# Kernel tuning notes

Hardware: AMD Instinct MI355X
Metric: run time of the kernel (lower is better)

The kernel has to match this reference:

```python
import jax, jax.numpy as jnp
import numpy as np

T, B = 512, 256
OBS, H = 64, 512
M1, M2 = 512, 256


def setup_inputs() -> dict:
    key = jax.random.key(0)
    k = jax.random.split(key, 10)
    n = lambda i, shape, s=1.0: jax.random.normal(k[i], shape, dtype=jnp.float32) * s
    return {
        "x": n(0, (T * B, OBS)),
        "done": (jax.random.uniform(k[1], (T * B,)) < 0.05).astype(jnp.float32),
        "h0": n(2, (1, B, H), 0.1),
        "c0": n(3, (1, B, H), 0.1),
        "W_ih": n(4, (4 * H, OBS), OBS ** -0.5),
        "W_hh": n(5, (4 * H, H), H ** -0.5),
        "b_ih": jnp.zeros((4 * H,), jnp.float32),
        "b_hh": jnp.zeros((4 * H,), jnp.float32),
        "ln_g": jnp.ones((H,), jnp.float32),
        "ln_b": jnp.zeros((H,), jnp.float32),
        "W1": n(6, (M1, H), H ** -0.5),
        "b1": jnp.zeros((M1,), jnp.float32),
        "W2": n(7, (M2, M1), M1 ** -0.5),
        "b2": jnp.zeros((M2,), jnp.float32),
        "Wv": n(8, (1, M2), M2 ** -0.5),
        "bv": jnp.zeros((1,), jnp.float32),
    }


def _forward(x, done, h0, c0, W_ih, W_hh, b_ih, b_hh, ln_g, ln_b, W1, b1, W2, b2, Wv, bv):
    Bsz = h0.shape[1]
    obs = W_ih.shape[1]
    xs = x.reshape(-1, Bsz, obs)   # [T, B, obs]
    ds = done.reshape(-1, Bsz)     # [T, B]

    def step(carry, td):
        h, c = carry
        xt, dt = td
        m = (1.0 - dt)[:, None]    # done-based state reset, as in LSTMwithDones
        h = h * m
        c = c * m
        gates = xt @ W_ih.T + b_ih + h @ W_hh.T + b_hh  # [B, 4H]
        i, f, g, o = jnp.split(gates, 4, axis=-1)       # torch gate order i,f,g,o
        c = jax.nn.sigmoid(f) * c + jax.nn.sigmoid(i) * jnp.tanh(g)
        h = jax.nn.sigmoid(o) * jnp.tanh(c)
        return (h, c), h

    (hT, cT), hs = jax.lax.scan(step, (h0[0], c0[0]), (xs, ds))
    hidden = hs.reshape(-1, hs.shape[-1])  # flatten(cat(new_hidden), 0, 1) -> [T*B, H]

    # LayerNorm (eps = 1e-5, torch default)
    mu = hidden.mean(-1, keepdims=True)
    var = ((hidden - mu) ** 2).mean(-1, keepdims=True)
    hidden = (hidden - mu) * jax.lax.rsqrt(var + 1e-5) * ln_g + ln_b

    # MLP with tanh activation after every Linear (build_mlp appends act each layer)
    hmlp = jnp.tanh(hidden @ W1.T + b1)
    hmlp = jnp.tanh(hmlp @ W2.T + b2)
    value = hmlp @ Wv.T + bv               # [T*B, 1]
    return value, hT[None], cT[None]


def reference(x, done, h0, c0, W_ih, W_hh, b_ih, b_hh, ln_g, ln_b, W1, b1, W2, b2, Wv, bv):
    return _forward(x, done, h0, c0, W_ih, W_hh, b_ih, b_hh, ln_g, ln_b, W1, b1, W2, b2, Wv, bv)
```

## Files before the change

kernel.cpp:

```cpp
#include <hip/hip_runtime.h>
#include <stdint.h>

constexpr int T_STEPS = 512;
constexpr int BSZ     = 256;
constexpr int OBSD    = 64;
constexpr int HID     = 512;
constexpr int NROWS   = T_STEPS * BSZ;

constexpr int GROUPS = 16;
constexpr int WPG    = 16;
constexpr int BW     = 16;

typedef __attribute__((ext_vector_type(8))) short bf16x8;
typedef __attribute__((ext_vector_type(4))) float f32x4;

__device__ __forceinline__ float bf2f(uint16_t u) {
  union { uint32_t i; float f; } v; v.i = ((uint32_t)u) << 16; return v.f;
}
__device__ __forceinline__ uint16_t f2bf(float f) {
  union { float f; uint32_t i; } v; v.f = f;
  return (uint16_t)((v.i + 0x7FFFu + ((v.i >> 16) & 1u)) >> 16);
}
__device__ __forceinline__ uint64_t pack4(float a, float b, float c, float d) {
  uint32_t lo = (uint32_t)f2bf(a) | ((uint32_t)f2bf(b) << 16);
  uint32_t hi = (uint32_t)f2bf(c) | ((uint32_t)f2bf(d) << 16);
  return (uint64_t)lo | ((uint64_t)hi << 32);
}
__device__ __forceinline__ float sigm(float x) { return 1.f / (1.f + __expf(-x)); }
__device__ __forceinline__ float tanh_fast(float x) {
  float e = __expf(2.f * x);
  return 1.f - 2.f / (e + 1.f);
}

__device__ __forceinline__ void gll16(const void* g, void* l) {
  __builtin_amdgcn_global_load_lds(
      (const __attribute__((address_space(1))) uint32_t*)g,
      (__attribute__((address_space(3))) uint32_t*)l, 16, 0, 0);
}

__global__ __launch_bounds__(256, 1) void lstm_kernel(
    const float* __restrict__ xin, const float* __restrict__ done,
    const float* __restrict__ h0, const float* __restrict__ c0,
    const float* __restrict__ W_ih, const float* __restrict__ W_hh,
    const float* __restrict__ b_ih, const float* __restrict__ b_hh,
    uint16_t* __restrict__ hs, uint32_t* __restrict__ flg,
    float* __restrict__ out)
{
  __shared__ char  Ab[16 * 1152];
  __shared__ float gl[4 * 528];
  __shared__ float bl[128];

  const int wg   = blockIdx.x;
  const int g    = wg & 15;
  const int win  = wg >> 4;
  const int bg   = g * BW;
  const int tid  = threadIdx.x;
  const int lane = tid & 63;
  const int q    = tid >> 6;

  __builtin_amdgcn_fence(__ATOMIC_ACQUIRE, "agent");

  bf16x8 bq0[18], bq1[18];
  {
    const int r0  = q * 512 + win * 32 + (lane & 15);
    const int r1  = r0 + 16;
    const int kg8 = (lane >> 4) * 8;
    #pragma unroll
    for (int ks = 0; ks < 18; ++ks) {
      const float* s0 = (ks < 16)
          ? (W_hh + (size_t)r0 * 512 + ks * 32 + kg8)
          : (W_ih + (size_t)r0 * 64 + (ks - 16) * 32 + kg8);
      const float* s1 = (ks < 16)
          ? (W_hh + (size_t)r1 * 512 + ks * 32 + kg8)
          : (W_ih + (size_t)r1 * 64 + (ks - 16) * 32 + kg8);
      float4 a0 = *(const float4*)s0;
      float4 a1 = *(const float4*)(s0 + 4);
      float4 b0 = *(const float4*)s1;
      float4 b1 = *(const float4*)(s1 + 4);
      bf16x8 va, vb;
      va[0] = (short)f2bf(a0.x); va[1] = (short)f2bf(a0.y);
      va[2] = (short)f2bf(a0.z); va[3] = (short)f2bf(a0.w);
      va[4] = (short)f2bf(a1.x); va[5] = (short)f2bf(a1.y);
      va[6] = (short)f2bf(a1.z); va[7] = (short)f2bf(a1.w);
      vb[0] = (short)f2bf(b0.x); vb[1] = (short)f2bf(b0.y);
      vb[2] = (short)f2bf(b0.z); vb[3] = (short)f2bf(b0.w);
      vb[4] = (short)f2bf(b1.x); vb[5] = (short)f2bf(b1.y);
      vb[6] = (short)f2bf(b1.z); vb[7] = (short)f2bf(b1.w);
      bq0[ks] = va; bq1[ks] = vb;
    }
  }
  if (tid < 128) {
    int gq = tid >> 5, c = tid & 31;
    int grow = gq * 512 + win * 32 + c;
    bl[tid] = b_ih[grow] + b_hh[grow];
  }

  const int b_loc = tid >> 4;
  const int n0    = (tid & 15) * 2;
  float creg0 = c0[(size_t)(bg + b_loc) * HID + win * 32 + n0];
  float creg1 = c0[(size_t)(bg + b_loc) * HID + win * 32 + n0 + 1];

  const int sr  = tid >> 4;
  const int sc4 = (tid & 15) * 4;
  const int rw  = q * 4;

  __syncthreads();

  for (int t = 0; t < T_STEPS; ++t) {
    const float* xp = xin + ((size_t)t * BSZ + bg + sr) * OBSD + sc4;
    float4 xa = *(const float4*)xp;
    float dvs[4];
    #pragma unroll
    for (int r8 = 0; r8 < 4; ++r8)
      dvs[r8] = done[(size_t)t * BSZ + bg + rw + r8];
    float dv_b = done[(size_t)t * BSZ + bg + b_loc];

    *(uint64_t*)(Ab + ((sr * 1152 + 1024 + sc4 * 2) ^ ((sr & 7) << 4))) =
        pack4(xa.x, xa.y, xa.z, xa.w);

    if (t > 0) {
      for (;;) {
        uint32_t f = (lane < WPG)
            ? __hip_atomic_load(flg + g * 64 + q * 16 + lane,
                                __ATOMIC_RELAXED, __HIP_MEMORY_SCOPE_AGENT)
            : 0xFFFFFFFFu;
        if (__all((int)(f >= (uint32_t)t))) break;
        __builtin_amdgcn_s_sleep(1);
      }
      __builtin_amdgcn_fence(__ATOMIC_ACQUIRE, "workgroup");
    }

    if (t == 0) {
      #pragma unroll
      for (int r8 = 0; r8 < 4; ++r8) {
        int r = rw + r8;
        uint64_t v0 = 0, v1 = 0;
        if (dvs[r8] <= 0.5f) {
          const float* hp = h0 + (size_t)(bg + r) * HID;
          float4 ha = *(const float4*)(hp + lane * 4);
          float4 hb = *(const float4*)(hp + 256 + lane * 4);
          v0 = pack4(ha.x, ha.y, ha.z, ha.w);
          v1 = pack4(hb.x, hb.y, hb.z, hb.w);
        }
        *(uint64_t*)(Ab + ((r * 1152 + lane * 8) ^ ((r & 7) << 4))) = v0;
        *(uint64_t*)(Ab + ((r * 1152 + 512 + lane * 8) ^ ((r & 7) << 4))) = v1;
      }
    } else {
      #pragma unroll
      for (int r8 = 0; r8 < 4; ++r8) {
        int r = rw + r8;
        const uint4* hrow =
            (const uint4*)(hs + ((size_t)(t - 1) * BSZ + bg + r) * 512);
        uint4 v = hrow[lane];
        if (dvs[r8] > 0.5f) { v.x = 0; v.y = 0; v.z = 0; v.w = 0; }
        *(uint4*)(Ab + ((r * 1152 + lane * 16) ^ ((r & 7) << 4))) = v;
      }
    }
    __syncthreads();

    f32x4 ac0 = {0.f, 0.f, 0.f, 0.f};
    f32x4 ac1 = {0.f, 0.f, 0.f, 0.f};
    {
      const int ar = lane & 15;
      const int kg = lane >> 4;
      #pragma unroll
      for (int ks = 0; ks < 18; ++ks) {
        int kb = (ks * 32 + kg * 8) * 2;
        bf16x8 a = *(const bf16x8*)(Ab + ((ar * 1152 + kb) ^ ((ar & 7) << 4)));
        ac0 = __builtin_amdgcn_mfma_f32_16x16x32_bf16(a, bq0[ks], ac0, 0, 0, 0);
        ac1 = __builtin_amdgcn_mfma_f32_16x16x32_bf16(a, bq1[ks], ac1, 0, 0, 0);
      }
    }
    {
      int c  = lane & 15;
      int rb = (lane >> 4) * 4;
      #pragma unroll
      for (int r = 0; r < 4; ++r) {
        gl[q * 528 + (rb + r) * 33 + c]      = ac0[r];
        gl[q * 528 + (rb + r) * 33 + 16 + c] = ac1[r];
      }
    }
    __syncthreads();

    {
      float m = dv_b > 0.5f ? 0.f : 1.f;
      float h0v, h1v;
      {
        float I = gl[b_loc * 33 + n0]          + bl[n0];
        float F = gl[528 + b_loc * 33 + n0]    + bl[32 + n0];
        float G = gl[1056 + b_loc * 33 + n0]   + bl[64 + n0];
        float O = gl[1584 + b_loc * 33 + n0]   + bl[96 + n0];
        float cc = creg0 * m;
        cc = sigm(F) * cc + sigm(I) * tanh_fast(G);
        creg0 = cc;
        h0v = sigm(O) * tanh_fast(cc);
      }
      {
        int n1 = n0 + 1;
        float I = gl[b_loc * 33 + n1]          + bl[n1];
        float F = gl[528 + b_loc * 33 + n1]    + bl[32 + n1];
        float G = gl[1056 + b_loc * 33 + n1]   + bl[64 + n1];
        float O = gl[1584 + b_loc * 33 + n1]   + bl[96 + n1];
        float cc = creg1 * m;
        cc = sigm(F) * cc + sigm(I) * tanh_fast(G);
        creg1 = cc;
        h1v = sigm(O) * tanh_fast(cc);
      }
      uint32_t pk = (uint32_t)f2bf(h0v) | ((uint32_t)f2bf(h1v) << 16);
      uint32_t* hp = (uint32_t*)(hs + ((size_t)t * BSZ + bg + b_loc) * HID + win * 32 + n0);
      __hip_atomic_store(hp, pk, __ATOMIC_RELAXED, __HIP_MEMORY_SCOPE_AGENT);
      if (t == T_STEPS - 1) {
        size_t ob = (size_t)(bg + b_loc) * HID + win * 32 + n0;
        out[NROWS + ob]         = h0v;
        out[NROWS + ob + 1]     = h1v;
        out[2 * NROWS + ob]     = creg0;
        out[2 * NROWS + ob + 1] = creg1;
      }
    }
    asm volatile("s_waitcnt vmcnt(0)" ::: "memory");
    if ((tid & 63) == 0)
      __hip_atomic_store(flg + g * 64 + q * 16 + win, (uint32_t)(t + 1),
                         __ATOMIC_RELAXED, __HIP_MEMORY_SCOPE_AGENT);
  }
}

__global__ void uv_kernel(const float* __restrict__ W1, const float* __restrict__ ln_g,
                          const float* __restrict__ ln_b, const float* __restrict__ b1,
                          float* __restrict__ u, float* __restrict__ v)
{
  const int lane = threadIdx.x & 63;
  const int row  = blockIdx.x * 4 + (threadIdx.x >> 6);
  const float* wp = W1 + (size_t)row * 512 + lane * 8;
  float4 w0 = *(const float4*)wp;
  float4 w1 = *(const float4*)(wp + 4);
  float4 g0 = *(const float4*)(ln_g + lane * 8);
  float4 g1 = *(const float4*)(ln_g + lane * 8 + 4);
  float4 b0 = *(const float4*)(ln_b + lane * 8);
  float4 b1v = *(const float4*)(ln_b + lane * 8 + 4);
  float su = b0.x * w0.x + b0.y * w0.y + b0.z * w0.z + b0.w * w0.w
           + b1v.x * w1.x + b1v.y * w1.y + b1v.z * w1.z + b1v.w * w1.w;
  float sv = g0.x * w0.x + g0.y * w0.y + g0.z * w0.z + g0.w * w0.w
           + g1.x * w1.x + g1.y * w1.y + g1.z * w1.z + g1.w * w1.w;
  #pragma unroll
  for (int o = 1; o < 64; o <<= 1) { su += __shfl_xor(su, o); sv += __shfl_xor(sv, o); }
  if (lane == 0) { u[row] = su + b1[row]; v[row] = sv; }
}

template<int MODE>
__global__ __launch_bounds__(256, 2) void gemm_fused(
    const uint16_t* __restrict__ Abase, const uint16_t* __restrict__ W,
    uint16_t* __restrict__ C, int ntiles,
    const float* __restrict__ uvec, const float* __restrict__ vvec,
    const float* __restrict__ bias)
{
  __shared__ uint16_t At[64 * 512];
  __shared__ float sRS[64];
  __shared__ float sMRS[64];
  const int tid  = threadIdx.x;
  const int lane = tid & 63;
  const int wv   = tid >> 6;
  const size_t mbase = (size_t)blockIdx.x * 64;

  for (int r8 = 0; r8 < 16; ++r8) {
    int row = wv * 16 + r8;
    int sb  = (lane * 16) ^ ((row & 7) << 4);
    gll16(Abase + (mbase + row) * 512 + sb / 2, At + row * 512);
  }
  __syncthreads();

  if constexpr (MODE == 0) {
    for (int r8 = 0; r8 < 16; ++r8) {
      int row = wv * 16 + r8;
      bf16x8 v = *(const bf16x8*)((const char*)At +
                                  ((row * 1024 + lane * 16) ^ ((row & 7) << 4)));
      float s = 0.f, s2 = 0.f;
      #pragma unroll
      for (int j = 0; j < 8; ++j) {
        float f = bf2f((uint16_t)v[j]);
        s += f; s2 += f * f;
      }
      #pragma unroll
      for (int o = 1; o < 64; o <<= 1) {
        s += __shfl_xor(s, o); s2 += __shfl_xor(s2, o);
      }
      if (lane == 0) {
        float mu  = s * (1.f / 512.f);
        float var = s2 * (1.f / 512.f) - mu * mu;
        float rs  = rsqrtf(var + 1e-5f);
        sRS[row]  = rs;
        sMRS[row] = mu * rs;
      }
    }
    __syncthreads();
  }

  const int fr = lane & 15, kg = lane >> 4;
  const int mloc = (wv & 1) * 32;
  const int nhalf = (wv >> 1) * 64;

  for (int nt = 0; nt < ntiles; ++nt) {
    const int nbase = nt * 128 + nhalf;
    f32x4 vz = {0.f, 0.f, 0.f, 0.f};
    f32x4 acc[4][2];
    #pragma unroll
    for (int i = 0; i < 4; ++i) { acc[i][0] = vz; acc[i][1] = vz; }

    #pragma unroll 4
    for (int kb = 0; kb < 16; ++kb) {
      const int ke = kb * 32 + kg * 8;
      bf16x8 wf[4];
      #pragma unroll
      for (int i = 0; i < 4; ++i)
        wf[i] = *(const bf16x8*)(W + (size_t)(nbase + i * 16 + fr) * 512 + ke);
      bf16x8 af[2];
      #pragma unroll
      for (int j = 0; j < 2; ++j) {
        int mr = mloc + j * 16 + fr;
        af[j] = *(const bf16x8*)((const char*)At + ((mr * 1024 + ke * 2) ^ ((mr & 7) << 4)));
      }
      #pragma unroll
      for (int i = 0; i < 4; ++i)
        #pragma unroll
        for (int j = 0; j < 2; ++j)
          acc[i][j] = __builtin_amdgcn_mfma_f32_16x16x32_bf16(wf[i], af[j], acc[i][j], 0, 0, 0);
    }

    #pragma unroll
    for (int j = 0; j < 2; ++j) {
      int ml = mloc + j * 16 + fr;
      size_t m = mbase + ml;
      float rs = 0.f, mrs = 0.f;
      if constexpr (MODE == 0) { rs = sRS[ml]; mrs = sMRS[ml]; }
      #pragma unroll
      for (int i = 0; i < 4; ++i) {
        int n = nbase + i * 16 + kg * 4;
        float o0, o1, o2, o3;
        if constexpr (MODE == 0) {
          float4 uu = *(const float4*)(uvec + n);
          float4 vv = *(const float4*)(vvec + n);
          o0 = tanh_fast(rs * acc[i][j][0] - mrs * vv.x + uu.x);
          o1 = tanh_fast(rs * acc[i][j][1] - mrs * vv.y + uu.y);
          o2 = tanh_fast(rs * acc[i][j][2] - mrs * vv.z + uu.z);
          o3 = tanh_fast(rs * acc[i][j][3] - mrs * vv.w + uu.w);
        } else {
          float4 bb = *(const float4*)(bias + n);
          o0 = tanh_fast(acc[i][j][0] + bb.x);
          o1 = tanh_fast(acc[i][j][1] + bb.y);
          o2 = tanh_fast(acc[i][j][2] + bb.z);
          o3 = tanh_fast(acc[i][j][3] + bb.w);
        }
        uint32_t lo = (uint32_t)f2bf(o0) | ((uint32_t)f2bf(o1) << 16);
        uint32_t hi = (uint32_t)f2bf(o2) | ((uint32_t)f2bf(o3) << 16);
        *(uint64_t*)(C + m * 512 + n) = (uint64_t)lo | ((uint64_t)hi << 32);
      }
    }
    __syncthreads();
  }
}

__global__ void gemv_kernel(const uint16_t* __restrict__ a2, const float* __restrict__ Wv,
                            const float* __restrict__ bv, float* __restrict__ outv)
{
  const int lane = threadIdx.x & 63;
  const size_t row = (size_t)blockIdx.x * 4 + (threadIdx.x >> 6);
  const uint16_t* p = a2 + row * 512 + lane * 4;
  uint64_t v = *(const uint64_t*)p;
  float4 w = *(const float4*)(Wv + lane * 4);
  float d = bf2f((uint16_t)(v & 0xFFFF)) * w.x
          + bf2f((uint16_t)((v >> 16) & 0xFFFF)) * w.y
          + bf2f((uint16_t)((v >> 32) & 0xFFFF)) * w.z
          + bf2f((uint16_t)((v >> 48) & 0xFFFF)) * w.w;
  #pragma unroll
  for (int o = 1; o < 64; o <<= 1) d += __shfl_xor(d, o);
  if (lane == 0) outv[row] = d + bv[0];
}

__global__ void wconv_kernel(const float* __restrict__ W1, const float* __restrict__ W2,
                             const float* __restrict__ ln_g, uint16_t* __restrict__ dst)
{
  int idx = blockIdx.x * 256 + threadIdx.x;
  int i4 = idx * 4;
  float4 v;
  if (i4 < 262144) {
    v = *(const float4*)(W1 + i4);
    int c = i4 & 511;
    float4 gv = *(const float4*)(ln_g + c);
    v.x *= gv.x; v.y *= gv.y; v.z *= gv.z; v.w *= gv.w;
  } else {
    v = *(const float4*)(W2 + (i4 - 262144));
  }
  uint32_t lo = (uint32_t)f2bf(v.x) | ((uint32_t)f2bf(v.y) << 16);
  uint32_t hi = (uint32_t)f2bf(v.z) | ((uint32_t)f2bf(v.w) << 16);
  *(uint64_t*)(dst + i4) = (uint64_t)lo | ((uint64_t)hi << 32);
}

extern "C" void kernel_launch(void* const* d_in, const int* in_sizes, int n_in,
                              void* d_out, int out_size, void* d_ws, size_t ws_size,
                              hipStream_t stream)
{
  (void)in_sizes; (void)n_in;
  const float* x    = (const float*)d_in[0];
  const float* done = (const float*)d_in[1];
  const float* h0   = (const float*)d_in[2];
  const float* c0   = (const float*)d_in[3];
  const float* W_ih = (const float*)d_in[4];
  const float* W_hh = (const float*)d_in[5];
  const float* b_ih = (const float*)d_in[6];
  const float* b_hh = (const float*)d_in[7];
  const float* ln_g = (const float*)d_in[8];
  const float* ln_b = (const float*)d_in[9];
  const float* W1   = (const float*)d_in[10];
  const float* b1   = (const float*)d_in[11];
  const float* W2   = (const float*)d_in[12];
  const float* b2   = (const float*)d_in[13];
  const float* Wv   = (const float*)d_in[14];
  const float* bv   = (const float*)d_in[15];
  float* out = (float*)d_out;
  char* ws = (char*)d_ws;

  constexpr size_t NEED = 2097152ULL + 134217728ULL;
  if (ws_size < NEED) {
    hipMemsetAsync(d_out, 0, (size_t)out_size * 4, stream);
    return;
  }
  uint32_t* flg  = (uint32_t*)ws;
  uint16_t* wbf  = (uint16_t*)(ws + 16384);
  float*    uv_u = (float*)(ws + 802816);
  float*    uv_v = (float*)(ws + 802816 + 2048);
  uint16_t* hsb  = (uint16_t*)(ws + 2097152);

  hipMemsetAsync(ws, 0, 16384, stream);
  hipLaunchKernelGGL(wconv_kernel, dim3(384), dim3(256), 0, stream, W1, W2, ln_g, wbf);
  hipLaunchKernelGGL(uv_kernel, dim3(128), dim3(256), 0, stream, W1, ln_g, ln_b, b1, uv_u, uv_v);
  hipLaunchKernelGGL(lstm_kernel, dim3(256), dim3(256), 0, stream,
                     x, done, h0, c0, W_ih, W_hh, b_ih, b_hh, hsb, flg, out);
  hipLaunchKernelGGL((gemm_fused<0>), dim3(2048), dim3(256), 0, stream,
                     hsb, wbf, hsb, 4, uv_u, uv_v, (const float*)nullptr);
  hipLaunchKernelGGL((gemm_fused<1>), dim3(2048), dim3(256), 0, stream,
                     hsb, wbf + 262144, hsb, 2,
                     (const float*)nullptr, (const float*)nullptr, b2);
  hipLaunchKernelGGL(gemv_kernel, dim3(32768), dim3(256), 0, stream, hsb, Wv, bv, out);
}
```

Baseline: 1.903 ms.

## Fuse value head into second MLP GEMM, merge prep kernels, drop spin sleep

The final value projection now happens inside the second MLP GEMM epilogue, via per-row partial dot products and a shared-memory reduction. This skips writing the second activation to global memory and the separate GEMV launch that read it back. The weight-conversion and u/v precompute kernels are merged into a single launch. The LSTM flag spin-wait no longer sleeps between polls, which can cut step latency but adds memory traffic from polling.

```diff
diff --git a/kernel.cpp b/kernel.cpp
--- a/kernel.cpp
+++ b/kernel.cpp
@@ -125,7 +125,6 @@
                                 __ATOMIC_RELAXED, __HIP_MEMORY_SCOPE_AGENT)
             : 0xFFFFFFFFu;
         if (__all((int)(f >= (uint32_t)t))) break;
-        __builtin_amdgcn_s_sleep(1);
       }
       __builtin_amdgcn_fence(__ATOMIC_ACQUIRE, "workgroup");
     }
@@ -224,34 +223,50 @@
   }
 }
 
-__global__ void uv_kernel(const float* __restrict__ W1, const float* __restrict__ ln_g,
-                          const float* __restrict__ ln_b, const float* __restrict__ b1,
-                          float* __restrict__ u, float* __restrict__ v)
+__global__ void prep_kernel(const float* __restrict__ W1, const float* __restrict__ W2,
+                            const float* __restrict__ ln_g, const float* __restrict__ ln_b,
+                            const float* __restrict__ b1, uint16_t* __restrict__ dst,
+                            float* __restrict__ u, float* __restrict__ v)
 {
-  const int lane = threadIdx.x & 63;
-  const int row  = blockIdx.x * 4 + (threadIdx.x >> 6);
-  const float* wp = W1 + (size_t)row * 512 + lane * 8;
-  float4 w0 = *(const float4*)wp;
-  float4 w1 = *(const float4*)(wp + 4);
-  float4 g0 = *(const float4*)(ln_g + lane * 8);
-  float4 g1 = *(const float4*)(ln_g + lane * 8 + 4);
-  float4 b0 = *(const float4*)(ln_b + lane * 8);
-  float4 b1v = *(const float4*)(ln_b + lane * 8 + 4);
-  float su = b0.x * w0.x + b0.y * w0.y + b0.z * w0.z + b0.w * w0.w
-           + b1v.x * w1.x + b1v.y * w1.y + b1v.z * w1.z + b1v.w * w1.w;
-  float sv = g0.x * w0.x + g0.y * w0.y + g0.z * w0.z + g0.w * w0.w
-           + g1.x * w1.x + g1.y * w1.y + g1.z * w1.z + g1.w * w1.w;
-  #pragma unroll
-  for (int o = 1; o < 64; o <<= 1) { su += __shfl_xor(su, o); sv += __shfl_xor(sv, o); }
-  if (lane == 0) { u[row] = su + b1[row]; v[row] = sv; }
-}
-
-template<int MODE>
-__global__ __launch_bounds__(256, 2) void gemm_fused(
+  if (blockIdx.x < 384) {
+    int idx = blockIdx.x * 256 + threadIdx.x;
+    int i4 = idx * 4;
+    float4 val;
+    if (i4 < 262144) {
+      val = *(const float4*)(W1 + i4);
+      int c = i4 & 511;
+      float4 gv = *(const float4*)(ln_g + c);
+      val.x *= gv.x; val.y *= gv.y; val.z *= gv.z; val.w *= gv.w;
+    } else {
+      val = *(const float4*)(W2 + (i4 - 262144));
+    }
+    uint32_t lo = (uint32_t)f2bf(val.x) | ((uint32_t)f2bf(val.y) << 16);
+    uint32_t hi = (uint32_t)f2bf(val.z) | ((uint32_t)f2bf(val.w) << 16);
+    *(uint64_t*)(dst + i4) = (uint64_t)lo | ((uint64_t)hi << 32);
+  } else {
+    const int lane = threadIdx.x & 63;
+    const int row  = (blockIdx.x - 384) * 4 + (threadIdx.x >> 6);
+    const float* wp = W1 + (size_t)row * 512 + lane * 8;
+    float4 w0 = *(const float4*)wp;
+    float4 w1 = *(const float4*)(wp + 4);
+    float4 g0 = *(const float4*)(ln_g + lane * 8);
+    float4 g1 = *(const float4*)(ln_g + lane * 8 + 4);
+    float4 b0 = *(const float4*)(ln_b + lane * 8);
+    float4 b1v = *(const float4*)(ln_b + lane * 8 + 4);
+    float su = b0.x * w0.x + b0.y * w0.y + b0.z * w0.z + b0.w * w0.w
+             + b1v.x * w1.x + b1v.y * w1.y + b1v.z * w1.z + b1v.w * w1.w;
+    float sv = g0.x * w0.x + g0.y * w0.y + g0.z * w0.z + g0.w * w0.w
+             + g1.x * w1.x + g1.y * w1.y + g1.z * w1.z + g1.w * w1.w;
+    #pragma unroll
+    for (int o = 1; o < 64; o <<= 1) { su += __shfl_xor(su, o); sv += __shfl_xor(sv, o); }
+    if (lane == 0) { u[row] = su + b1[row]; v[row] = sv; }
+  }
+}
+
+__global__ __launch_bounds__(256, 2) void gemm1_kernel(
     const uint16_t* __restrict__ Abase, const uint16_t* __restrict__ W,
-    uint16_t* __restrict__ C, int ntiles,
-    const float* __restrict__ uvec, const float* __restrict__ vvec,
-    const float* __restrict__ bias)
+    uint16_t* __restrict__ C,
+    const float* __restrict__ uvec, const float* __restrict__ vvec)
 {
   __shared__ uint16_t At[64 * 512];
   __shared__ float sRS[64];
@@ -268,37 +283,35 @@
   }
   __syncthreads();
 
-  if constexpr (MODE == 0) {
-    for (int r8 = 0; r8 < 16; ++r8) {
-      int row = wv * 16 + r8;
-      bf16x8 v = *(const bf16x8*)((const char*)At +
-                                  ((row * 1024 + lane * 16) ^ ((row & 7) << 4)));
-      float s = 0.f, s2 = 0.f;
-      #pragma unroll
-      for (int j = 0; j < 8; ++j) {
-        float f = bf2f((uint16_t)v[j]);
-        s += f; s2 += f * f;
-      }
-      #pragma unroll
-      for (int o = 1; o < 64; o <<= 1) {
-        s += __shfl_xor(s, o); s2 += __shfl_xor(s2, o);
-      }
-      if (lane == 0) {
-        float mu  = s * (1.f / 512.f);
-        float var = s2 * (1.f / 512.f) - mu * mu;
-        float rs  = rsqrtf(var + 1e-5f);
-        sRS[row]  = rs;
-        sMRS[row] = mu * rs;
-      }
-    }
-    __syncthreads();
-  }
+  for (int r8 = 0; r8 < 16; ++r8) {
+    int row = wv * 16 + r8;
+    bf16x8 v = *(const bf16x8*)((const char*)At +
+                                ((row * 1024 + lane * 16) ^ ((row & 7) << 4)));
+    float s = 0.f, s2 = 0.f;
+    #pragma unroll
+    for (int j = 0; j < 8; ++j) {
+      float f = bf2f((uint16_t)v[j]);
+      s += f; s2 += f * f;
+    }
+    #pragma unroll
+    for (int o = 1; o < 64; o <<= 1) {
+      s += __shfl_xor(s, o); s2 += __shfl_xor(s2, o);
+    }
+    if (lane == 0) {
+      float mu  = s * (1.f / 512.f);
+      float var = s2 * (1.f / 512.f) - mu * mu;
+      float rs  = rsqrtf(var + 1e-5f);
+      sRS[row]  = rs;
+      sMRS[row] = mu * rs;
+    }
+  }
+  __syncthreads();
 
   const int fr = lane & 15, kg = lane >> 4;
   const int mloc = (wv & 1) * 32;
   const int nhalf = (wv >> 1) * 64;
 
-  for (int nt = 0; nt < ntiles; ++nt) {
+  for (int nt = 0; nt < 4; ++nt) {
     const int nbase = nt * 128 + nhalf;
     f32x4 vz = {0.f, 0.f, 0.f, 0.f};
     f32x4 acc[4][2];
@@ -329,26 +342,16 @@
     for (int j = 0; j < 2; ++j) {
       int ml = mloc + j * 16 + fr;
       size_t m = mbase + ml;
-      float rs = 0.f, mrs = 0.f;
-      if constexpr (MODE == 0) { rs = sRS[ml]; mrs = sMRS[ml]; }
+      float rs = sRS[ml], mrs = sMRS[ml];
       #pragma unroll
       for (int i = 0; i < 4; ++i) {
         int n = nbase + i * 16 + kg * 4;
-        float o0, o1, o2, o3;
-        if constexpr (MODE == 0) {
-          float4 uu = *(const float4*)(uvec + n);
-          float4 vv = *(const float4*)(vvec + n);
-          o0 = tanh_fast(rs * acc[i][j][0] - mrs * vv.x + uu.x);
-          o1 = tanh_fast(rs * acc[i][j][1] - mrs * vv.y + uu.y);
-          o2 = tanh_fast(rs * acc[i][j][2] - mrs * vv.z + uu.z);
-          o3 = tanh_fast(rs * acc[i][j][3] - mrs * vv.w + uu.w);
-        } else {
-          float4 bb = *(const float4*)(bias + n);
-          o0 = tanh_fast(acc[i][j][0] + bb.x);
-          o1 = tanh_fast(acc[i][j][1] + bb.y);
-          o2 = tanh_fast(acc[i][j][2] + bb.z);
-          o3 = tanh_fast(acc[i][j][3] + bb.w);
-        }
+        float4 uu = *(const float4*)(uvec + n);
+        float4 vv = *(const float4*)(vvec + n);
+        float o0 = tanh_fast(rs * acc[i][j][0] - mrs * vv.x + uu.x);
+        float o1 = tanh_fast(rs * acc[i][j][1] - mrs * vv.y + uu.y);
+        float o2 = tanh_fast(rs * acc[i][j][2] - mrs * vv.z + uu.z);
+        float o3 = tanh_fast(rs * acc[i][j][3] - mrs * vv.w + uu.w);
         uint32_t lo = (uint32_t)f2bf(o0) | ((uint32_t)f2bf(o1) << 16);
         uint32_t hi = (uint32_t)f2bf(o2) | ((uint32_t)f2bf(o3) << 16);
         *(uint64_t*)(C + m * 512 + n) = (uint64_t)lo | ((uint64_t)hi << 32);
@@ -358,40 +361,85 @@
   }
 }
 
-__global__ void gemv_kernel(const uint16_t* __restrict__ a2, const float* __restrict__ Wv,
-                            const float* __restrict__ bv, float* __restrict__ outv)
+__global__ __launch_bounds__(256, 2) void gemm2_value_kernel(
+    const uint16_t* __restrict__ Abase, const uint16_t* __restrict__ W,
+    const float* __restrict__ bias, const float* __restrict__ Wv,
+    const float* __restrict__ bv, float* __restrict__ outv)
 {
-  const int lane = threadIdx.x & 63;
-  const size_t row = (size_t)blockIdx.x * 4 + (threadIdx.x >> 6);
-  const uint16_t* p = a2 + row * 512 + lane * 4;
-  uint64_t v = *(const uint64_t*)p;
-  float4 w = *(const float4*)(Wv + lane * 4);
-  float d = bf2f((uint16_t)(v & 0xFFFF)) * w.x
-          + bf2f((uint16_t)((v >> 16) & 0xFFFF)) * w.y
-          + bf2f((uint16_t)((v >> 32) & 0xFFFF)) * w.z
-          + bf2f((uint16_t)((v >> 48) & 0xFFFF)) * w.w;
+  __shared__ uint16_t At[64 * 512];
+  __shared__ float vred[2][64];
+  const int tid  = threadIdx.x;
+  const int lane = tid & 63;
+  const int wv   = tid >> 6;
+  const size_t mbase = (size_t)blockIdx.x * 64;
+
+  for (int r8 = 0; r8 < 16; ++r8) {
+    int row = wv * 16 + r8;
+    int sb  = (lane * 16) ^ ((row & 7) << 4);
+    gll16(Abase + (mbase + row) * 512 + sb / 2, At + row * 512);
+  }
+  __syncthreads();
+
+  const int fr = lane & 15, kg = lane >> 4;
+  const int mloc = (wv & 1) * 32;
+  const int nhalf = (wv >> 1) * 64;
+
+  float vpart0 = 0.f, vpart1 = 0.f;
+
   #pragma unroll
-  for (int o = 1; o < 64; o <<= 1) d += __shfl_xor(d, o);
-  if (lane == 0) outv[row] = d + bv[0];
-}
-
-__global__ void wconv_kernel(const float* __restrict__ W1, const float* __restrict__ W2,
-                             const float* __restrict__ ln_g, uint16_t* __restrict__ dst)
-{
-  int idx = blockIdx.x * 256 + threadIdx.x;
-  int i4 = idx * 4;
-  float4 v;
-  if (i4 < 262144) {
-    v = *(const float4*)(W1 + i4);
-    int c = i4 & 511;
-    float4 gv = *(const float4*)(ln_g + c);
-    v.x *= gv.x; v.y *= gv.y; v.z *= gv.z; v.w *= gv.w;
-  } else {
-    v = *(const float4*)(W2 + (i4 - 262144));
-  }
-  uint32_t lo = (uint32_t)f2bf(v.x) | ((uint32_t)f2bf(v.y) << 16);
-  uint32_t hi = (uint32_t)f2bf(v.z) | ((uint32_t)f2bf(v.w) << 16);
-  *(uint64_t*)(dst + i4) = (uint64_t)lo | ((uint64_t)hi << 32);
+  for (int nt = 0; nt < 2; ++nt) {
+    const int nbase = nt * 128 + nhalf;
+    f32x4 vz = {0.f, 0.f, 0.f, 0.f};
+    f32x4 acc[4][2];
+    #pragma unroll
+    for (int i = 0; i < 4; ++i) { acc[i][0] = vz; acc[i][1] = vz; }
+
+    #pragma unroll 4
+    for (int kb = 0; kb < 16; ++kb) {
+      const int ke = kb * 32 + kg * 8;
+      bf16x8 wf[4];
+      #pragma unroll
+      for (int i = 0; i < 4; ++i)
+        wf[i] = *(const bf16x8*)(W + (size_t)(nbase + i * 16 + fr) * 512 + ke);
+      bf16x8 af[2];
+      #pragma unroll
+      for (int j = 0; j < 2; ++j) {
+        int mr = mloc + j * 16 + fr;
+        af[j] = *(const bf16x8*)((const char*)At + ((mr * 1024 + ke * 2) ^ ((mr & 7) << 4)));
+      }
+      #pragma unroll
+      for (int i = 0; i < 4; ++i)
+        #pragma unroll
+        for (int j = 0; j < 2; ++j)
+          acc[i][j] = __builtin_amdgcn_mfma_f32_16x16x32_bf16(wf[i], af[j], acc[i][j], 0, 0, 0);
+    }
+
+    #pragma unroll
+    for (int j = 0; j < 2; ++j) {
+      float vp = 0.f;
+      #pragma unroll
+      for (int i = 0; i < 4; ++i) {
+        int n = nbase + i * 16 + kg * 4;
+        float4 bb  = *(const float4*)(bias + n);
+        float4 wv4 = *(const float4*)(Wv + n);
+        vp += tanh_fast(acc[i][j][0] + bb.x) * wv4.x
+            + tanh_fast(acc[i][j][1] + bb.y) * wv4.y
+            + tanh_fast(acc[i][j][2] + bb.z) * wv4.z
+            + tanh_fast(acc[i][j][3] + bb.w) * wv4.w;
+      }
+      if (j == 0) vpart0 += vp; else vpart1 += vp;
+    }
+  }
+
+  vpart0 += __shfl_xor(vpart0, 16); vpart0 += __shfl_xor(vpart0, 32);
+  vpart1 += __shfl_xor(vpart1, 16); vpart1 += __shfl_xor(vpart1, 32);
+  if (kg == 0) {
+    vred[wv >> 1][mloc + fr]      = vpart0;
+    vred[wv >> 1][mloc + 16 + fr] = vpart1;
+  }
+  __syncthreads();
+  if (tid < 64)
+    outv[mbase + tid] = vred[0][tid] + vred[1][tid] + bv[0];
 }
 
 extern "C" void kernel_launch(void* const* d_in, const int* in_sizes, int n_in,
@@ -430,14 +478,12 @@
   uint16_t* hsb  = (uint16_t*)(ws + 2097152);
 
   hipMemsetAsync(ws, 0, 16384, stream);
-  hipLaunchKernelGGL(wconv_kernel, dim3(384), dim3(256), 0, stream, W1, W2, ln_g, wbf);
-  hipLaunchKernelGGL(uv_kernel, dim3(128), dim3(256), 0, stream, W1, ln_g, ln_b, b1, uv_u, uv_v);
+  hipLaunchKernelGGL(prep_kernel, dim3(512), dim3(256), 0, stream,
+                     W1, W2, ln_g, ln_b, b1, wbf, uv_u, uv_v);
   hipLaunchKernelGGL(lstm_kernel, dim3(256), dim3(256), 0, stream,
                      x, done, h0, c0, W_ih, W_hh, b_ih, b_hh, hsb, flg, out);
-  hipLaunchKernelGGL((gemm_fused<0>), dim3(2048), dim3(256), 0, stream,
-                     hsb, wbf, hsb, 4, uv_u, uv_v, (const float*)nullptr);
-  hipLaunchKernelGGL((gemm_fused<1>), dim3(2048), dim3(256), 0, stream,
-                     hsb, wbf + 262144, hsb, 2,
-                     (const float*)nullptr, (const float*)nullptr, b2);
-  hipLaunchKernelGGL(gemv_kernel, dim3(32768), dim3(256), 0, stream, hsb, Wv, bv, out);
-}
+  hipLaunchKernelGGL(gemm1_kernel, dim3(2048), dim3(256), 0, stream,
+                     hsb, wbf, hsb, uv_u, uv_v);
+  hipLaunchKernelGGL(gemm2_value_kernel, dim3(2048), dim3(256), 0, stream,
+                     hsb, wbf + 262144, b2, Wv, bv, out);
+}
```

Result: faster. 1.865 ms (-2.0%).
